# Kernel optimization log

Measured on AMD Instinct MI355X. Metric: run time of the kernel, lower is better.

Reference implementation:

```python
import jax, jax.numpy as jnp
import numpy as np
from jax import lax

FORGET_BIAS = 1.0
EPS = 1e-12


def l2_normalize_time(x):
    # tf.nn.l2_normalize(x, dim=1): normalize over the timestep axis
    sq = jnp.sum(jnp.square(x), axis=1, keepdims=True)
    return x * lax.rsqrt(jnp.maximum(sq, EPS))


def lstm_layer(x, W, b, units):
    """TF LSTMCell: kernel (in+units, 4*units), gates split as i, j, f, o.
    x: [B, T, D] -> [B, T, units]"""
    B = x.shape[0]

    def step(carry, xt):
        c, h = carry
        z = jnp.concatenate([xt, h], axis=-1) @ W + b  # [B, 4*units]
        i, j, f, o = jnp.split(z, 4, axis=-1)
        c = jax.nn.sigmoid(f + FORGET_BIAS) * c + jax.nn.sigmoid(i) * jnp.tanh(j)
        h = jax.nn.sigmoid(o) * jnp.tanh(c)
        return (c, h), h

    init = (jnp.zeros((B, units), x.dtype), jnp.zeros((B, units), x.dtype))
    _, hs = lax.scan(step, init, jnp.swapaxes(x, 0, 1))  # [T, B, units]
    return jnp.swapaxes(hs, 0, 1)


def setup_inputs() -> dict:
    key = jax.random.key(0)
    ks = jax.random.split(key, 5)
    B, T, U = 256, 2048, 64
    x = jax.random.normal(ks[0], (B, T, 1), dtype=jnp.float32)
    # layer 0: LSTMCell(64), input dim 1 -> kernel (1+64, 4*64)
    W0 = jax.random.normal(ks[1], (1 + U, 4 * U), dtype=jnp.float32) * 0.05
    b0 = jnp.zeros((4 * U,), dtype=jnp.float32)
    # layer 1: LSTMCell(1), input dim 64 -> kernel (64+1, 4)
    W1 = jax.random.normal(ks[2], (U + 1, 4), dtype=jnp.float32) * 0.05
    b1 = jnp.zeros((4,), dtype=jnp.float32)
    # dense(1)
    Wd = jax.random.normal(ks[3], (1, 1), dtype=jnp.float32)
    bd = jnp.zeros((1,), dtype=jnp.float32)
    return {"x": x, "W0": W0, "b0": b0, "W1": W1, "b1": b1, "Wd": Wd, "bd": bd}


def reference(x, W0, b0, W1, b1, Wd, bd):
    h = l2_normalize_time(x)          # [B, T, 1]
    h = lstm_layer(h, W0, b0, 64)     # [B, T, 64]
    h = lstm_layer(h, W1, b1, 1)      # [B, T, 1]
    out = h @ Wd + bd                 # dense(1), no activation
    return out
```

## Files before the change

kernel.cpp:

```cpp
#include <hip/hip_runtime.h>
#include <math.h>

#define TT 2048
#define UU 64
#define BB 256
#define NTHR 192

typedef float v2f __attribute__((ext_vector_type(2)));
typedef float v4f __attribute__((ext_vector_type(4)));

__device__ __forceinline__ float frcp(float x) { return __builtin_amdgcn_rcpf(x); }
__device__ __forceinline__ float fsigmoid(float x) { return frcp(1.0f + __expf(-x)); }
__device__ __forceinline__ float ftanh(float x) { return 1.0f - 2.0f * frcp(1.0f + __expf(2.0f * x)); }

__device__ __forceinline__ void pkfma_ll(v2f& a, v2f h, v2f w) {
    asm("v_pk_fma_f32 %0, %1, %2, %0 op_sel:[0,0,0] op_sel_hi:[0,1,1]"
        : "+v"(a) : "v"(h), "v"(w));
}
__device__ __forceinline__ void pkfma_hh(v2f& a, v2f h, v2f w) {
    asm("v_pk_fma_f32 %0, %1, %2, %0 op_sel:[1,0,0] op_sel_hi:[1,1,1]"
        : "+v"(a) : "v"(h), "v"(w));
}

__global__
__attribute__((amdgpu_flat_work_group_size(NTHR, NTHR)))
__attribute__((amdgpu_waves_per_eu(1, 1)))
void lstm_ts_kernel(
    const float* __restrict__ x, const float* __restrict__ W0,
    const float* __restrict__ b0, const float* __restrict__ W1,
    const float* __restrict__ b1, const float* __restrict__ Wd,
    const float* __restrict__ bd, float* __restrict__ out)
{
    __shared__ __align__(16) float xbuf[TT];
    __shared__ __align__(16) float ringS0[2][UU];
    __shared__ __align__(16) float ringS1[2][UU];
    __shared__ __align__(16) v2f zb0[UU];
    __shared__ __align__(16) v2f zb1[UU];
    __shared__ float red[3];

    const int tid = threadIdx.x;
    const int wid = tid >> 6;
    const int u = tid & 63;
    const int b = blockIdx.x;
    const float* xrow = x + b * TT;
    float* outrow = out + b * TT;

    float ss = 0.f;
    for (int i = tid; i < TT; i += NTHR) {
        float v = xrow[i];
        xbuf[i] = v;
        ss += v * v;
    }
    #pragma unroll
    for (int m = 1; m < 64; m <<= 1) ss += __shfl_xor(ss, m, 64);
    if (u == 0) red[wid] = ss;
    if (wid < 2) {
        (wid == 0 ? ringS0 : ringS1)[1][u] = 0.f;
    }
    __syncthreads();

    if (wid < 2) {
        const int go = wid * 128;
        const float sq = (red[0] + red[1]) + red[2];
        const float scale = 1.0f / sqrtf(fmaxf(sq, 1e-12f));

        #define DECLW(k) v2f WP##k; { const float* r_ = W0 + (1 + (k)) * 256 + go; \
            WP##k.x = r_[u]; WP##k.y = r_[64 + u]; } \
            asm volatile("" : "+v"(WP##k));
        DECLW(0)  DECLW(1)  DECLW(2)  DECLW(3)  DECLW(4)  DECLW(5)  DECLW(6)  DECLW(7)
        DECLW(8)  DECLW(9)  DECLW(10) DECLW(11) DECLW(12) DECLW(13) DECLW(14) DECLW(15)
        DECLW(16) DECLW(17) DECLW(18) DECLW(19) DECLW(20) DECLW(21) DECLW(22) DECLW(23)
        DECLW(24) DECLW(25) DECLW(26) DECLW(27) DECLW(28) DECLW(29) DECLW(30) DECLW(31)
        DECLW(32) DECLW(33) DECLW(34) DECLW(35) DECLW(36) DECLW(37) DECLW(38) DECLW(39)
        DECLW(40) DECLW(41) DECLW(42) DECLW(43) DECLW(44) DECLW(45) DECLW(46) DECLW(47)
        DECLW(48) DECLW(49) DECLW(50) DECLW(51) DECLW(52) DECLW(53) DECLW(54) DECLW(55)
        DECLW(56) DECLW(57) DECLW(58) DECLW(59) DECLW(60) DECLW(61) DECLW(62) DECLW(63)
        #undef DECLW

        const float wxa = W0[go + u] * scale;
        const float wxb = W0[go + 64 + u] * scale;
        const float bca = b0[go + u], bcb = b0[go + 64 + u];

        float (*myring)[UU] = (wid == 0) ? ringS0 : ringS1;
        v2f* zbme = (wid == 0) ? zb0 : zb1;
        v2f* zbot = (wid == 0) ? zb1 : zb0;

        float c0 = 0.f;

        for (int t = 0; t < TT; ++t) {
            const float xr = xbuf[t];
            const float* hs = myring[(t + 1) & 1];

            v2f a0, a1 = 0.f, a2 = 0.f, a3 = 0.f;
            a0.x = fmaf(xr, wxa, bca); a0.y = fmaf(xr, wxb, bcb);

            #define MAC4(m, Wa, Wb, Wc, Wd_) { \
                v4f hv_ = *(const v4f*)(hs + 4 * (m)); \
                v2f h01_ = __builtin_shufflevector(hv_, hv_, 0, 1); \
                v2f h23_ = __builtin_shufflevector(hv_, hv_, 2, 3); \
                pkfma_ll(a0, h01_, Wa); pkfma_hh(a1, h01_, Wb); \
                pkfma_ll(a2, h23_, Wc); pkfma_hh(a3, h23_, Wd_); \
            }
            MAC4(0,  WP0,  WP1,  WP2,  WP3)
            MAC4(1,  WP4,  WP5,  WP6,  WP7)
            MAC4(2,  WP8,  WP9,  WP10, WP11)
            MAC4(3,  WP12, WP13, WP14, WP15)
            MAC4(4,  WP16, WP17, WP18, WP19)
            MAC4(5,  WP20, WP21, WP22, WP23)
            MAC4(6,  WP24, WP25, WP26, WP27)
            MAC4(7,  WP28, WP29, WP30, WP31)
            MAC4(8,  WP32, WP33, WP34, WP35)
            MAC4(9,  WP36, WP37, WP38, WP39)
            MAC4(10, WP40, WP41, WP42, WP43)
            MAC4(11, WP44, WP45, WP46, WP47)
            MAC4(12, WP48, WP49, WP50, WP51)
            MAC4(13, WP52, WP53, WP54, WP55)
            MAC4(14, WP56, WP57, WP58, WP59)
            MAC4(15, WP60, WP61, WP62, WP63)
            #undef MAC4

            const v2f zown = (a0 + a1) + (a2 + a3);
            zbme[u] = zown;
            __syncthreads();

            const v2f zoth = zbot[u];
            const v2f zij = (wid == 0) ? zown : zoth;
            const v2f zfo = (wid == 0) ? zoth : zown;

            c0 = fsigmoid(zfo.x + 1.0f) * c0 + fsigmoid(zij.x) * ftanh(zij.y);
            const float h = fsigmoid(zfo.y) * ftanh(c0);

            myring[t & 1][u] = h;
        }
        __syncthreads();
    } else {
        const float w1v0 = W1[u * 4 + 0], w1v1 = W1[u * 4 + 1];
        const float w1v2 = W1[u * 4 + 2], w1v3 = W1[u * 4 + 3];
        const float w1h0 = W1[256], w1h1 = W1[257], w1h2 = W1[258], w1h3 = W1[259];
        const float b10 = b1[0], b11 = b1[1], b12 = b1[2], b13 = b1[3];
        const float wd = Wd[0], bdv = bd[0];

        float c1 = 0.f, h1 = 0.f, oval = 0.f;

        #define L1STEP(s) { \
            const float hu = ringS0[(s) & 1][u];   \
            float p0 = hu * w1v0, p1 = hu * w1v1, p2 = hu * w1v2, p3 = hu * w1v3; \
            _Pragma("unroll") \
            for (int m = 1; m < 64; m <<= 1) { \
                p0 += __shfl_xor(p0, m, 64); \
                p1 += __shfl_xor(p1, m, 64); \
                p2 += __shfl_xor(p2, m, 64); \
                p3 += __shfl_xor(p3, m, 64); \
            } \
            const float z1i = p0 + fmaf(h1, w1h0, b10); \
            const float z1j = p1 + fmaf(h1, w1h1, b11); \
            const float z1f = p2 + fmaf(h1, w1h2, b12); \
            const float z1o = p3 + fmaf(h1, w1h3, b13); \
            c1 = fsigmoid(z1f + 1.0f) * c1 + fsigmoid(z1i) * ftanh(z1j); \
            h1 = fsigmoid(z1o) * ftanh(c1); \
            const float ov = fmaf(h1, wd, bdv); \
            if (((s) & 63) == u) oval = ov; \
            if (((s) & 63) == 63) outrow[((s) & ~63) + u] = oval; \
        }

        for (int t = 0; t < TT; ++t) {
            __syncthreads();
            if (t > 0) L1STEP(t - 1)
        }
        __syncthreads();
        L1STEP(TT - 1)
        #undef L1STEP
    }
}

extern "C" void kernel_launch(void* const* d_in, const int* in_sizes, int n_in,
                              void* d_out, int out_size, void* d_ws, size_t ws_size,
                              hipStream_t stream) {
    const float* x  = (const float*)d_in[0];
    const float* W0 = (const float*)d_in[1];
    const float* b0 = (const float*)d_in[2];
    const float* W1 = (const float*)d_in[3];
    const float* b1 = (const float*)d_in[4];
    const float* Wd = (const float*)d_in[5];
    const float* bd = (const float*)d_in[6];
    float* out = (float*)d_out;
    lstm_ts_kernel<<<BB, NTHR, 0, stream>>>(x, W0, b0, W1, b1, Wd, bd, out);
}
```

Baseline: 999.1 us.

## Pack two batch sequences per workgroup with six waves per block

```diff
diff --git a/kernel.cpp b/kernel.cpp
--- a/kernel.cpp
+++ b/kernel.cpp
@@ -3,8 +3,8 @@
 
 #define TT 2048
 #define UU 64
-#define BB 256
-#define NTHR 192
+#define NBLK 128
+#define NTHR 384
 
 typedef float v2f __attribute__((ext_vector_type(2)));
 typedef float v4f __attribute__((ext_vector_type(4)));
@@ -24,44 +24,47 @@
 
 __global__
 __attribute__((amdgpu_flat_work_group_size(NTHR, NTHR)))
-__attribute__((amdgpu_waves_per_eu(1, 1)))
+__attribute__((amdgpu_waves_per_eu(2, 2)))
 void lstm_ts_kernel(
     const float* __restrict__ x, const float* __restrict__ W0,
     const float* __restrict__ b0, const float* __restrict__ W1,
     const float* __restrict__ b1, const float* __restrict__ Wd,
     const float* __restrict__ bd, float* __restrict__ out)
 {
-    __shared__ __align__(16) float xbuf[TT];
-    __shared__ __align__(16) float ringS0[2][UU];
-    __shared__ __align__(16) float ringS1[2][UU];
-    __shared__ __align__(16) v2f zb0[UU];
-    __shared__ __align__(16) v2f zb1[UU];
-    __shared__ float red[3];
+    __shared__ __align__(16) float xbuf[2][TT];
+    __shared__ __align__(16) float ringS0[2][2][UU];
+    __shared__ __align__(16) float ringS1[2][2][UU];
+    __shared__ __align__(16) v2f zb0[2][UU];
+    __shared__ __align__(16) v2f zb1[2][UU];
+    __shared__ float red[2][3];
 
     const int tid = threadIdx.x;
     const int wid = tid >> 6;
     const int u = tid & 63;
-    const int b = blockIdx.x;
+    const int eid = (wid >= 3) ? 1 : 0;
+    const int wl = wid - 3 * eid;
+    const int b = 2 * blockIdx.x + eid;
     const float* xrow = x + b * TT;
     float* outrow = out + b * TT;
 
     float ss = 0.f;
-    for (int i = tid; i < TT; i += NTHR) {
+    const int ltid = wl * 64 + u;
+    for (int i = ltid; i < TT; i += 192) {
         float v = xrow[i];
-        xbuf[i] = v;
+        xbuf[eid][i] = v;
         ss += v * v;
     }
     #pragma unroll
     for (int m = 1; m < 64; m <<= 1) ss += __shfl_xor(ss, m, 64);
-    if (u == 0) red[wid] = ss;
-    if (wid < 2) {
-        (wid == 0 ? ringS0 : ringS1)[1][u] = 0.f;
+    if (u == 0) red[eid][wl] = ss;
+    if (wl < 2) {
+        (wl == 0 ? ringS0 : ringS1)[eid][1][u] = 0.f;
     }
     __syncthreads();
 
-    if (wid < 2) {
-        const int go = wid * 128;
-        const float sq = (red[0] + red[1]) + red[2];
+    if (wl < 2) {
+        const int go = wl * 128;
+        const float sq = (red[eid][0] + red[eid][1]) + red[eid][2];
         const float scale = 1.0f / sqrtf(fmaxf(sq, 1e-12f));
 
         #define DECLW(k) v2f WP##k; { const float* r_ = W0 + (1 + (k)) * 256 + go; \
@@ -81,14 +84,14 @@
         const float wxb = W0[go + 64 + u] * scale;
         const float bca = b0[go + u], bcb = b0[go + 64 + u];
 
-        float (*myring)[UU] = (wid == 0) ? ringS0 : ringS1;
-        v2f* zbme = (wid == 0) ? zb0 : zb1;
-        v2f* zbot = (wid == 0) ? zb1 : zb0;
+        float (*myring)[UU] = (wl == 0) ? ringS0[eid] : ringS1[eid];
+        v2f* zbme = (wl == 0) ? zb0[eid] : zb1[eid];
+        v2f* zbot = (wl == 0) ? zb1[eid] : zb0[eid];
 
         float c0 = 0.f;
 
         for (int t = 0; t < TT; ++t) {
-            const float xr = xbuf[t];
+            const float xr = xbuf[eid][t];
             const float* hs = myring[(t + 1) & 1];
 
             v2f a0, a1 = 0.f, a2 = 0.f, a3 = 0.f;
@@ -124,8 +127,8 @@
             __syncthreads();
 
             const v2f zoth = zbot[u];
-            const v2f zij = (wid == 0) ? zown : zoth;
-            const v2f zfo = (wid == 0) ? zoth : zown;
+            const v2f zij = (wl == 0) ? zown : zoth;
+            const v2f zfo = (wl == 0) ? zoth : zown;
 
             c0 = fsigmoid(zfo.x + 1.0f) * c0 + fsigmoid(zij.x) * ftanh(zij.y);
             const float h = fsigmoid(zfo.y) * ftanh(c0);
@@ -143,7 +146,7 @@
         float c1 = 0.f, h1 = 0.f, oval = 0.f;
 
         #define L1STEP(s) { \
-            const float hu = ringS0[(s) & 1][u];   \
+            const float hu = ringS0[eid][(s) & 1][u];   \
             float p0 = hu * w1v0, p1 = hu * w1v1, p2 = hu * w1v2, p3 = hu * w1v3; \
             _Pragma("unroll") \
             for (int m = 1; m < 64; m <<= 1) { \
@@ -184,5 +187,5 @@
     const float* Wd = (const float*)d_in[5];
     const float* bd = (const float*)d_in[6];
     float* out = (float*)d_out;
-    lstm_ts_kernel<<<BB, NTHR, 0, stream>>>(x, W0, b0, W1, b1, Wd, bd, out);
+    lstm_ts_kernel<<<NBLK, NTHR, 0, stream>>>(x, W0, b0, W1, b1, Wd, bd, out);
 }
```

After: 1.273 ms. +27.4%, slower.
